# Optimization experiments

Hardware: AMD Instinct MI355X
Metric: run time of the kernel (lower is better)

## Reference

```python
import jax, jax.numpy as jnp
import numpy as np

D_MODEL = 1024
N_LAYERS = 4
EXPAND = 2
D_CONV = 4
D_STATE = 16
INTER = EXPAND * D_MODEL          # 2048
DT_RANK = (D_MODEL + 15) // 16    # 64, HF: math.ceil(d_model/16)
B_SZ = 4
SEQ = 1024
EPS = 1e-5


def setup_inputs() -> dict:
    key = jax.random.key(0)
    ks = jax.random.split(key, 8)
    nrm = lambda k, s: (0.02 * jax.random.normal(k, s)).astype(jnp.float32)
    return {
        "x": jax.random.normal(ks[0], (B_SZ, SEQ, D_MODEL), dtype=jnp.float32),
        "in_w": nrm(ks[1], (N_LAYERS, 2 * INTER, D_MODEL)),           # in_proj (no bias)
        "conv_w": nrm(ks[2], (N_LAYERS, INTER, D_CONV)),              # depthwise conv weight
        "conv_b": jnp.zeros((N_LAYERS, INTER), jnp.float32),           # conv bias
        "x_w": nrm(ks[3], (N_LAYERS, DT_RANK + 2 * D_STATE, INTER)),  # x_proj (no bias)
        "dt_w": nrm(ks[4], (N_LAYERS, INTER, DT_RANK)),               # dt_proj weight
        "dt_b": jax.random.uniform(ks[5], (N_LAYERS, INTER), minval=-4.0, maxval=-2.0).astype(jnp.float32),
        "A_log": jnp.tile(jnp.log(jnp.arange(1, D_STATE + 1, dtype=jnp.float32)), (N_LAYERS, INTER, 1)),
        "D": jnp.ones((N_LAYERS, INTER), jnp.float32),
        "out_w": nrm(ks[6], (N_LAYERS, D_MODEL, INTER)),              # out_proj (no bias)
        "norm_w": jnp.ones((N_LAYERS, D_MODEL), jnp.float32),          # per-block RMSNorm
        "norm_f_w": jnp.ones((D_MODEL,), jnp.float32),                 # final RMSNorm
    }


def _rmsnorm(x, w):
    return x * jax.lax.rsqrt(jnp.mean(x * x, axis=-1, keepdims=True) + EPS) * w


def _mixer(x, in_w, conv_w, conv_b, x_w, dt_w, dt_b, A_log, Dp, out_w):
    # x: [B, L, d_model]
    Bb = x.shape[0]
    proj = x @ in_w.T                              # [B, L, 2I]
    hs, gate = jnp.split(proj, 2, axis=-1)          # each [B, L, I]
    # causal depthwise conv over time
    hc = hs.transpose(0, 2, 1)                      # [B, I, L]
    hc = jnp.pad(hc, ((0, 0), (0, 0), (D_CONV - 1, 0)))
    hc = jax.lax.conv_general_dilated(
        hc, conv_w[:, None, :], (1,), 'VALID',
        dimension_numbers=('NCH', 'OIH', 'NCH'), feature_group_count=INTER)
    hc = hc + conv_b[None, :, None]
    u = jax.nn.silu(hc).transpose(0, 2, 1)          # [B, L, I]
    ssm = u @ x_w.T                                 # [B, L, dt_rank + 2N]
    dt, Bm, Cm = jnp.split(ssm, [DT_RANK, DT_RANK + D_STATE], axis=-1)
    dt = jax.nn.softplus(dt @ dt_w.T + dt_b)        # [B, L, I]
    A = -jnp.exp(A_log)                             # [I, N]

    def step(state, xs):
        dt_t, B_t, C_t, u_t = xs                    # [B,I], [B,N], [B,N], [B,I]
        dA = jnp.exp(dt_t[:, :, None] * A[None])    # [B, I, N]
        state = dA * state + (dt_t * u_t)[:, :, None] * B_t[:, None, :]
        y = jnp.einsum('bin,bn->bi', state, C_t)
        return state, y

    init = jnp.zeros((Bb, INTER, D_STATE), x.dtype)
    xs = (dt.transpose(1, 0, 2), Bm.transpose(1, 0, 2),
          Cm.transpose(1, 0, 2), u.transpose(1, 0, 2))
    _, ys = jax.lax.scan(step, init, xs)            # ys: [L, B, I]
    y = ys.transpose(1, 0, 2) + u * Dp              # skip term D * u
    y = y * jax.nn.silu(gate)
    return y @ out_w.T                              # [B, L, d_model]


def reference(x, in_w, conv_w, conv_b, x_w, dt_w, dt_b, A_log, D, out_w, norm_w, norm_f_w):
    h = x
    for l in range(N_LAYERS):
        h = h + _mixer(_rmsnorm(h, norm_w[l]), in_w[l], conv_w[l], conv_b[l],
                       x_w[l], dt_w[l], dt_b[l], A_log[l], D[l], out_w[l])
    return _rmsnorm(h, norm_f_w)
```

## Files before the change

kernel.cpp:

```cpp
#include <hip/hip_runtime.h>
#include <hip/hip_bf16.h>
#include <math.h>

#define D_MODEL 1024
#define N_LAYERS 4
#define INTER 2048
#define D_CONV 4
#define D_STATE 16
#define DT_RANK 64
#define B_SZ 4
#define SEQ 1024
#define TOK (B_SZ*SEQ)
#define XROWS 128
#define EPSV 1e-5f
#define GCH 32
#define TC (SEQ/GCH)
#define KSPL 4

typedef unsigned short u16;
typedef __attribute__((ext_vector_type(8))) short bf16x8;
typedef __attribute__((ext_vector_type(4))) short s16x4;
typedef __attribute__((ext_vector_type(4))) float f32x4;

__device__ __forceinline__ u16 f2b(float f) {
    union { float f; unsigned u; } v; v.f = f;
    unsigned r = v.u + 0x7fffu + ((v.u >> 16) & 1u);
    return (u16)(r >> 16);
}
__device__ __forceinline__ float b2f(u16 h) {
    union { unsigned u; float f; } v; v.u = ((unsigned)h) << 16;
    return v.f;
}
__device__ __forceinline__ float silu(float x) {
    return x / (1.f + __expf(-x));
}
__device__ __forceinline__ void gload16(const void* g, void* l) {
    __builtin_amdgcn_global_load_lds(
        (const __attribute__((address_space(1))) void*)g,
        (__attribute__((address_space(3))) void*)l, 16, 0, 0);
}

__global__ __launch_bounds__(512, 2)
void gemm256_k(const u16* __restrict__ A, const u16* __restrict__ B,
               u16* __restrict__ C, int K, int ldc)
{
    __shared__ u16 lds[2][2][256 * 64];
    const int tid  = threadIdx.x;
    const int lane = tid & 63;
    const int wid  = tid >> 6;
    const int wr   = wid >> 2;
    const int wc   = wid & 3;
    const int row0 = blockIdx.y * 256;
    const int col0 = blockIdx.x * 256;
    const int r16   = lane & 15;
    const int khalf = lane >> 4;

    auto stage = [&](int buf, int k0) {
#pragma unroll
        for (int l = 0; l < 8; ++l) {
            int op = l >> 2;
            int c  = tid + (l & 3) * 512;
            int r  = c >> 3;
            int ds = c & 7;
            int sc = (ds ^ (r & 7)) * 8;
            const u16* src = op ? &B[(size_t)(col0 + r) * K + k0 + sc]
                                : &A[(size_t)(row0 + r) * K + k0 + sc];
            gload16(src, &lds[buf][op][c * 8]);
        }
    };
    auto rdA = [&](int buf, int mrow, int ks) -> bf16x8 {
        int row  = wr * 128 + mrow + r16;
        int phys = ((ks << 2) | khalf) ^ (row & 7);
        return *(const bf16x8*)&lds[buf][0][row * 64 + phys * 8];
    };
    auto rdB = [&](int buf, int nrow, int ks) -> bf16x8 {
        int row  = wc * 64 + nrow + r16;
        int phys = ((ks << 2) | khalf) ^ (row & 7);
        return *(const bf16x8*)&lds[buf][1][row * 64 + phys * 8];
    };

    f32x4 acc[8][4];
#pragma unroll
    for (int m = 0; m < 8; ++m)
#pragma unroll
        for (int n = 0; n < 4; ++n)
            acc[m][n] = (f32x4)0.f;

    bf16x8 af[4][2], bf2[2][2];

#define PHASE_MFMA(MH, NH, VMDRAIN) do {                                      \
    asm volatile("s_waitcnt lgkmcnt(0)" ::: "memory");                        \
    __builtin_amdgcn_sched_barrier(0);                                        \
    __builtin_amdgcn_s_setprio(1);                                            \
    _Pragma("unroll")                                                         \
    for (int ks = 0; ks < 2; ++ks)                                            \
        _Pragma("unroll")                                                     \
        for (int m = 0; m < 4; ++m)                                           \
            _Pragma("unroll")                                                 \
            for (int n = 0; n < 2; ++n)                                       \
                acc[(MH)*4+m][(NH)*2+n] =                                     \
                    __builtin_amdgcn_mfma_f32_16x16x32_bf16(                  \
                        af[m][ks], bf2[n][ks], acc[(MH)*4+m][(NH)*2+n],0,0,0);\
    __builtin_amdgcn_s_setprio(0);                                            \
    if (VMDRAIN) { asm volatile("s_waitcnt vmcnt(0)" ::: "memory"); }         \
    __builtin_amdgcn_s_barrier();                                             \
} while (0)

    const int nt = K >> 6;
    stage(0, 0);
    asm volatile("s_waitcnt vmcnt(0)" ::: "memory");
    __builtin_amdgcn_s_barrier();

    for (int j = 0; j < nt; ++j) {
        const int buf = j & 1;
        if (j + 1 < nt) stage(buf ^ 1, (j + 1) << 6);
#pragma unroll
        for (int m = 0; m < 4; ++m) {
            af[m][0] = rdA(buf, m * 16, 0); af[m][1] = rdA(buf, m * 16, 1);
        }
#pragma unroll
        for (int n = 0; n < 2; ++n) {
            bf2[n][0] = rdB(buf, n * 16, 0); bf2[n][1] = rdB(buf, n * 16, 1);
        }
        __builtin_amdgcn_s_barrier();
        PHASE_MFMA(0, 0, 0);
#pragma unroll
        for (int n = 0; n < 2; ++n) {
            bf2[n][0] = rdB(buf, 32 + n * 16, 0); bf2[n][1] = rdB(buf, 32 + n * 16, 1);
        }
        __builtin_amdgcn_s_barrier();
        PHASE_MFMA(0, 1, 0);
#pragma unroll
        for (int m = 0; m < 4; ++m) {
            af[m][0] = rdA(buf, 64 + m * 16, 0); af[m][1] = rdA(buf, 64 + m * 16, 1);
        }
        __builtin_amdgcn_s_barrier();
        PHASE_MFMA(1, 1, 0);
#pragma unroll
        for (int n = 0; n < 2; ++n) {
            bf2[n][0] = rdB(buf, n * 16, 0); bf2[n][1] = rdB(buf, n * 16, 1);
        }
        __builtin_amdgcn_s_barrier();
        PHASE_MFMA(1, 0, 1);
    }
#undef PHASE_MFMA

    const int orow = row0 + wr * 128;
    const int ocol = col0 + wc * 64;
#pragma unroll
    for (int am = 0; am < 8; ++am)
#pragma unroll
        for (int an = 0; an < 4; ++an)
#pragma unroll
            for (int r = 0; r < 4; ++r) {
                int rr = orow + am * 16 + khalf * 4 + r;
                int cc = ocol + an * 16 + r16;
                C[(size_t)rr * ldc + cc] = f2b(acc[am][an][r]);
            }
}

template<int EPI>
__global__ __launch_bounds__(256)
void gemm_bt(const u16* __restrict__ A, const u16* __restrict__ B,
             void* __restrict__ C, const float* __restrict__ aux,
             int K, int lda, int ldc)
{
    __shared__ u16 As[3][128 * 32];
    __shared__ u16 Bs[3][128 * 32];
    const int tid  = threadIdx.x;
    const int lane = tid & 63;
    const int w    = tid >> 6;
    const int wr   = w >> 1, wc = w & 1;
    const int row0 = blockIdx.y * 128;
    int col0 = blockIdx.x * 128;
    if (EPI == 4) {
        int part = blockIdx.x;
        col0 = 0;
        A += (size_t)part * K;
        B += (size_t)part * K;
        C = (void*)((float*)C + (size_t)part * TOK * XROWS);
    }
    const int r16   = lane & 15;
    const int khalf = lane >> 4;
    const int kslot = khalf ^ ((r16 >> 1) & 3);

    auto stage = [&](int buf, int k0) {
#pragma unroll
        for (int c = 0; c < 2; ++c) {
            int chunk = tid + c * 256;
            int r  = chunk >> 2;
            int j  = chunk & 3;
            int k8 = (j ^ ((r >> 1) & 3)) * 8;
            gload16(&A[(size_t)(row0 + r) * lda + k0 + k8], &As[buf][chunk * 8]);
            gload16(&B[(size_t)(col0 + r) * lda + k0 + k8], &Bs[buf][chunk * 8]);
        }
    };

    f32x4 acc[4][4];
#pragma unroll
    for (int m = 0; m < 4; ++m)
#pragma unroll
        for (int n = 0; n < 4; ++n)
            acc[m][n] = (f32x4)0.f;

    const int nt = K >> 5;
    stage(0, 0);
    if (nt > 1) stage(1, 32);

    int cur = 0, sb = 2;
    for (int t = 0; t < nt; ++t) {
        if (t + 2 < nt) {
            stage(sb, (t + 2) << 5);
            asm volatile("s_waitcnt vmcnt(8)" ::: "memory");
        } else if (t + 1 < nt) {
            asm volatile("s_waitcnt vmcnt(4)" ::: "memory");
        } else {
            asm volatile("s_waitcnt vmcnt(0)" ::: "memory");
        }
        __builtin_amdgcn_s_barrier();

        bf16x8 af[4], bfr[4];
#pragma unroll
        for (int m = 0; m < 4; ++m)
            af[m]  = *(const bf16x8*)&As[cur][(wr * 64 + m * 16 + r16) * 32 + kslot * 8];
#pragma unroll
        for (int n = 0; n < 4; ++n)
            bfr[n] = *(const bf16x8*)&Bs[cur][(wc * 64 + n * 16 + r16) * 32 + kslot * 8];
#pragma unroll
        for (int m = 0; m < 4; ++m)
#pragma unroll
            for (int n = 0; n < 4; ++n)
                acc[m][n] = __builtin_amdgcn_mfma_f32_16x16x32_bf16(
                    af[m], bfr[n], acc[m][n], 0, 0, 0);

        __builtin_amdgcn_sched_barrier(0);
        asm volatile("s_waitcnt lgkmcnt(0)" ::: "memory");
        __builtin_amdgcn_s_barrier();
        cur = (cur == 2) ? 0 : cur + 1;
        sb  = (sb  == 2) ? 0 : sb  + 1;
    }

    const int orow = row0 + wr * 64;
    const int ocol = col0 + wc * 64;
#pragma unroll
    for (int m = 0; m < 4; ++m)
#pragma unroll
        for (int n = 0; n < 4; ++n) {
#pragma unroll
            for (int r = 0; r < 4; ++r) {
                int rr = orow + m * 16 + khalf * 4 + r;
                int cc = ocol + n * 16 + r16;
                float v = acc[m][n][r];
                size_t o = (size_t)rr * ldc + cc;
                if (EPI == 0 || EPI == 4) {
                    ((float*)C)[o] = v;
                } else if (EPI == 2) {
                    float x = v + aux[cc];
                    float sp = (x > 20.f) ? x : log1pf(__expf(x));
                    ((u16*)C)[o] = f2b(sp);
                } else {
                    ((float*)C)[o] = aux[o] + v;
                }
            }
        }
}

__global__ __launch_bounds__(256)
void xred_k(const float* __restrict__ part, float* __restrict__ ssm,
            u16* __restrict__ dtr)
{
    int idx = blockIdx.x * 256 + threadIdx.x;
    int row = idx >> 5;
    int col = (idx & 31) * 4;
    size_t o = (size_t)row * XROWS + col;
    const size_t stride = (size_t)TOK * XROWS;
    f32x4 v = *(const f32x4*)&part[o];
#pragma unroll
    for (int p = 1; p < KSPL; ++p)
        v += *(const f32x4*)&part[o + p * stride];
    *(f32x4*)&ssm[o] = v;
    if (col < DT_RANK) {
        s16x4 d;
#pragma unroll
        for (int j = 0; j < 4; ++j) d[j] = (short)f2b(v[j]);
        *(s16x4*)&dtr[(size_t)row * DT_RANK + col] = d;
    }
}

template<int OUTBF>
__global__ __launch_bounds__(256)
void rmsnorm_k(const float* __restrict__ in, const float* __restrict__ w,
               void* __restrict__ out)
{
    __shared__ float red[4];
    const int row = blockIdx.x;
    const int tid = threadIdx.x;
    const float* r = in + (size_t)row * D_MODEL;
    f32x4 v = *(const f32x4*)&r[tid * 4];
    float ss = v[0]*v[0] + v[1]*v[1] + v[2]*v[2] + v[3]*v[3];
#pragma unroll
    for (int m = 32; m >= 1; m >>= 1) ss += __shfl_xor(ss, m, 64);
    if ((tid & 63) == 0) red[tid >> 6] = ss;
    __syncthreads();
    if (tid == 0) {
        float s = red[0] + red[1] + red[2] + red[3];
        red[0] = rsqrtf(s / (float)D_MODEL + EPSV);
    }
    __syncthreads();
    float sc = red[0];
    if (OUTBF) {
        u16* o = (u16*)out + (size_t)row * D_MODEL + tid * 4;
#pragma unroll
        for (int j = 0; j < 4; ++j) o[j] = f2b(v[j] * sc * w[tid * 4 + j]);
    } else {
        float* o = (float*)out + (size_t)row * D_MODEL + tid * 4;
#pragma unroll
        for (int j = 0; j < 4; ++j) o[j] = v[j] * sc * w[tid * 4 + j];
    }
}

__global__ __launch_bounds__(256)
void conv_silu_k(const u16* __restrict__ projbf, const float* __restrict__ w,
                 const float* __restrict__ bias, u16* __restrict__ ubf)
{
    const int row = blockIdx.x;
    const int t   = row & (SEQ - 1);
    const int i0  = threadIdx.x * 8;
    float acc[8];
    {
        f32x4 b0 = *(const f32x4*)&bias[i0];
        f32x4 b1 = *(const f32x4*)&bias[i0 + 4];
#pragma unroll
        for (int j = 0; j < 4; ++j) { acc[j] = b0[j]; acc[j + 4] = b1[j]; }
    }
    f32x4 wv[8];
#pragma unroll
    for (int j = 0; j < 8; ++j)
        wv[j] = *(const f32x4*)&w[(i0 + j) * 4];
#pragma unroll
    for (int k = 0; k < 4; ++k) {
        int tt = t - 3 + k;
        if (tt >= 0) {
            bf16x8 hv = *(const bf16x8*)&projbf[(size_t)(row - 3 + k) * 4096 + i0];
#pragma unroll
            for (int j = 0; j < 8; ++j)
                acc[j] += b2f((u16)hv[j]) * wv[j][k];
        }
    }
    bf16x8 o;
#pragma unroll
    for (int j = 0; j < 8; ++j)
        o[j] = (short)f2b(silu(acc[j]));
    *(bf16x8*)&ubf[(size_t)row * INTER + i0] = o;
}

__global__ __launch_bounds__(256)
void scan1_k(const u16* __restrict__ dtbf, const u16* __restrict__ ubf,
             const float* __restrict__ ssm, const float* __restrict__ Alog,
             float* __restrict__ cst, float* __restrict__ dts)
{
    __shared__ float Bs[TC][D_STATE];
    const int tid = threadIdx.x;
    const int i   = blockIdx.x * 256 + tid;
    const int g   = blockIdx.y;
    const int b   = blockIdx.z;
    const int t0  = g * TC;
    for (int idx = tid * 4; idx < TC * D_STATE; idx += 1024) {
        int t = idx >> 4, n = idx & 15;
        *(f32x4*)&Bs[t][n] =
            *(const f32x4*)&ssm[(size_t)(b * SEQ + t0 + t) * XROWS + DT_RANK + n];
    }
    __syncthreads();

    float a[D_STATE];
#pragma unroll
    for (int n = 0; n < D_STATE; ++n)
        a[n] = -__expf(Alog[(size_t)i * D_STATE + n]);

    float s[D_STATE];
#pragma unroll
    for (int n = 0; n < D_STATE; ++n) s[n] = 0.f;
    float dsum = 0.f;

    const u16* dtp = dtbf + (size_t)(b * SEQ + t0) * INTER + i;
    const u16* up  = ubf  + (size_t)(b * SEQ + t0) * INTER + i;
#pragma unroll 2
    for (int t = 0; t < TC; ++t) {
        float dt = b2f(dtp[(size_t)t * INTER]);
        float u  = b2f(up[(size_t)t * INTER]);
        float du = dt * u;
        dsum += dt;
        f32x4 B0 = *(const f32x4*)&Bs[t][0];
        f32x4 B1 = *(const f32x4*)&Bs[t][4];
        f32x4 B2 = *(const f32x4*)&Bs[t][8];
        f32x4 B3 = *(const f32x4*)&Bs[t][12];
#pragma unroll
        for (int n = 0; n < 4; ++n) {
            s[n]      = __expf(dt * a[n])      * s[n]      + du * B0[n];
            s[n + 4]  = __expf(dt * a[n + 4])  * s[n + 4]  + du * B1[n];
            s[n + 8]  = __expf(dt * a[n + 8])  * s[n + 8]  + du * B2[n];
            s[n + 12] = __expf(dt * a[n + 12]) * s[n + 12] + du * B3[n];
        }
    }
    size_t o = ((size_t)(b * GCH + g) * INTER + i) * D_STATE;
#pragma unroll
    for (int n = 0; n < D_STATE; n += 4) {
        f32x4 v = { s[n], s[n+1], s[n+2], s[n+3] };
        *(f32x4*)&cst[o + n] = v;
    }
    dts[(size_t)(b * GCH + g) * INTER + i] = dsum;
}

__global__ __launch_bounds__(256)
void scan2_k(float* __restrict__ cst, const float* __restrict__ dts,
             const float* __restrict__ Alog)
{
    int idx = blockIdx.x * 256 + threadIdx.x;
    int sub = idx & 3;
    int i   = (idx >> 2) & (INTER - 1);
    int b   = idx >> 13;
    int n0  = sub * 4;
    float a[4];
#pragma unroll
    for (int n = 0; n < 4; ++n)
        a[n] = -__expf(Alog[(size_t)i * D_STATE + n0 + n]);
    f32x4 s = (f32x4)0.f;
    for (int g = 0; g < GCH; ++g) {
        size_t o = ((size_t)(b * GCH + g) * INTER + i) * D_STATE + n0;
        f32x4 tmp = *(const f32x4*)&cst[o];
        *(f32x4*)&cst[o] = s;
        float d = dts[(size_t)(b * GCH + g) * INTER + i];
#pragma unroll
        for (int n = 0; n < 4; ++n)
            s[n] = __expf(a[n] * d) * s[n] + tmp[n];
    }
}

__global__ __launch_bounds__(256)
void scan3_k(const u16* __restrict__ dtbf, const u16* __restrict__ ubf,
             const float* __restrict__ ssm, const u16* __restrict__ projbf,
             const float* __restrict__ Alog, const float* __restrict__ Dp,
             const float* __restrict__ sst, u16* __restrict__ ybf)
{
    __shared__ float Bs[TC][D_STATE];
    __shared__ float Cs[TC][D_STATE];
    const int tid = threadIdx.x;
    const int i   = blockIdx.x * 256 + tid;
    const int g   = blockIdx.y;
    const int b   = blockIdx.z;
    const int t0  = g * TC;
    for (int idx = tid * 4; idx < TC * D_STATE; idx += 1024) {
        int t = idx >> 4, n = idx & 15;
        size_t row = (size_t)(b * SEQ + t0 + t) * XROWS;
        *(f32x4*)&Bs[t][n] = *(const f32x4*)&ssm[row + DT_RANK + n];
        *(f32x4*)&Cs[t][n] = *(const f32x4*)&ssm[row + DT_RANK + D_STATE + n];
    }
    __syncthreads();

    float a[D_STATE];
#pragma unroll
    for (int n = 0; n < D_STATE; ++n)
        a[n] = -__expf(Alog[(size_t)i * D_STATE + n]);
    const float Di = Dp[i];

    float s[D_STATE];
    size_t so = ((size_t)(b * GCH + g) * INTER + i) * D_STATE;
#pragma unroll
    for (int n = 0; n < D_STATE; n += 4) {
        f32x4 v = *(const f32x4*)&sst[so + n];
        s[n] = v[0]; s[n+1] = v[1]; s[n+2] = v[2]; s[n+3] = v[3];
    }

    const u16* dtp = dtbf   + (size_t)(b * SEQ + t0) * INTER + i;
    const u16* up  = ubf    + (size_t)(b * SEQ + t0) * INTER + i;
    const u16* gp  = projbf + (size_t)(b * SEQ + t0) * 4096 + INTER + i;
    u16*       yp  = ybf    + (size_t)(b * SEQ + t0) * INTER + i;
#pragma unroll 2
    for (int t = 0; t < TC; ++t) {
        float dt = b2f(dtp[(size_t)t * INTER]);
        float u  = b2f(up[(size_t)t * INTER]);
        float gt = b2f(gp[(size_t)t * 4096]);
        float du = dt * u;
        f32x4 B0 = *(const f32x4*)&Bs[t][0];
        f32x4 B1 = *(const f32x4*)&Bs[t][4];
        f32x4 B2 = *(const f32x4*)&Bs[t][8];
        f32x4 B3 = *(const f32x4*)&Bs[t][12];
        f32x4 C0 = *(const f32x4*)&Cs[t][0];
        f32x4 C1 = *(const f32x4*)&Cs[t][4];
        f32x4 C2 = *(const f32x4*)&Cs[t][8];
        f32x4 C3 = *(const f32x4*)&Cs[t][12];
        float y = 0.f;
#pragma unroll
        for (int n = 0; n < 4; ++n) {
            s[n]      = __expf(dt * a[n])      * s[n]      + du * B0[n];
            s[n + 4]  = __expf(dt * a[n + 4])  * s[n + 4]  + du * B1[n];
            s[n + 8]  = __expf(dt * a[n + 8])  * s[n + 8]  + du * B2[n];
            s[n + 12] = __expf(dt * a[n + 12]) * s[n + 12] + du * B3[n];
            y += s[n] * C0[n] + s[n + 4] * C1[n] + s[n + 8] * C2[n] + s[n + 12] * C3[n];
        }
        yp[(size_t)t * INTER] = f2b((y + Di * u) * silu(gt));
    }
}

__global__ __launch_bounds__(256)
void cvt_f2b_k(const float* __restrict__ in, u16* __restrict__ out, int n)
{
    int idx = blockIdx.x * 256 + threadIdx.x;
    if (idx < n) out[idx] = f2b(in[idx]);
}

__global__ __launch_bounds__(256)
void pad_xw_k(const float* __restrict__ xw, u16* __restrict__ out)
{
    int idx = blockIdx.x * 256 + threadIdx.x;
    if (idx >= N_LAYERS * XROWS * INTER) return;
    int l = idx / (XROWS * INTER);
    int r = (idx >> 11) & (XROWS - 1);
    int c = idx & (INTER - 1);
    out[idx] = (r < 96) ? f2b(xw[((size_t)l * 96 + r) * INTER + c]) : (u16)0;
}

extern "C" void kernel_launch(void* const* d_in, const int* in_sizes, int n_in,
                              void* d_out, int out_size, void* d_ws, size_t ws_size,
                              hipStream_t stream)
{
    const float* x      = (const float*)d_in[0];
    const float* in_w   = (const float*)d_in[1];
    const float* conv_w = (const float*)d_in[2];
    const float* conv_b = (const float*)d_in[3];
    const float* x_w    = (const float*)d_in[4];
    const float* dt_w   = (const float*)d_in[5];
    const float* dt_b   = (const float*)d_in[6];
    const float* A_log  = (const float*)d_in[7];
    const float* Dp     = (const float*)d_in[8];
    const float* out_w  = (const float*)d_in[9];
    const float* norm_w = (const float*)d_in[10];
    const float* norm_f = (const float*)d_in[11];

    char* ws = (char*)d_ws;
    size_t off = 0;
    auto alloc = [&](size_t bytes) { char* p = ws + off; off += (bytes + 255) & ~(size_t)255; return p; };

    u16*   inw_bf  = (u16*)  alloc((size_t)N_LAYERS * 4096 * 1024 * 2);
    u16*   xw_bf   = (u16*)  alloc((size_t)N_LAYERS * XROWS * INTER * 2);
    u16*   dtw_bf  = (u16*)  alloc((size_t)N_LAYERS * INTER * DT_RANK * 2);
    u16*   outw_bf = (u16*)  alloc((size_t)N_LAYERS * D_MODEL * INTER * 2);
    float* h       = (float*)alloc((size_t)TOK * D_MODEL * 4);
    u16*   xn_bf   = (u16*)  alloc((size_t)TOK * D_MODEL * 2);
    u16*   proj_bf = (u16*)  alloc((size_t)TOK * 4096 * 2);
    u16*   u_bf    = (u16*)  alloc((size_t)TOK * INTER * 2);
    float* ssm     = (float*)alloc((size_t)TOK * XROWS * 4);
    float* ssm_p   = (float*)alloc((size_t)KSPL * TOK * XROWS * 4);
    u16*   dtr_bf  = (u16*)  alloc((size_t)TOK * DT_RANK * 2);
    u16*   dt_bf   = (u16*)  alloc((size_t)TOK * INTER * 2);
    u16*   y_bf    = (u16*)  alloc((size_t)TOK * INTER * 2);
    float* cst     = (float*)alloc((size_t)B_SZ * GCH * INTER * D_STATE * 4);
    float* dts     = (float*)alloc((size_t)B_SZ * GCH * INTER * 4);
    (void)ws_size; (void)n_in; (void)in_sizes; (void)out_size;

    {
        int n = N_LAYERS * 4096 * 1024;
        cvt_f2b_k<<<n / 256, 256, 0, stream>>>(in_w, inw_bf, n);
        int np = N_LAYERS * XROWS * INTER;
        pad_xw_k<<<np / 256, 256, 0, stream>>>(x_w, xw_bf);
        int nd = N_LAYERS * INTER * DT_RANK;
        cvt_f2b_k<<<nd / 256, 256, 0, stream>>>(dt_w, dtw_bf, nd);
        int no = N_LAYERS * D_MODEL * INTER;
        cvt_f2b_k<<<no / 256, 256, 0, stream>>>(out_w, outw_bf, no);
    }

    hipMemcpyAsync(h, x, (size_t)TOK * D_MODEL * 4, hipMemcpyDeviceToDevice, stream);

    for (int l = 0; l < N_LAYERS; ++l) {
        rmsnorm_k<1><<<TOK, 256, 0, stream>>>(h, norm_w + (size_t)l * D_MODEL, xn_bf);
        gemm256_k<<<dim3(16, 16), 512, 0, stream>>>(
            xn_bf, inw_bf + (size_t)l * 4096 * 1024, proj_bf, 1024, 4096);
        conv_silu_k<<<TOK, 256, 0, stream>>>(
            proj_bf, conv_w + (size_t)l * INTER * D_CONV, conv_b + (size_t)l * INTER, u_bf);
        gemm_bt<4><<<dim3(KSPL, 32), 256, 0, stream>>>(
            u_bf, xw_bf + (size_t)l * XROWS * INTER, ssm_p, nullptr,
            INTER / KSPL, INTER, XROWS);
        xred_k<<<(TOK * 32) / 256, 256, 0, stream>>>(ssm_p, ssm, dtr_bf);
        gemm_bt<2><<<dim3(16, 32), 256, 0, stream>>>(
            dtr_bf, dtw_bf + (size_t)l * INTER * DT_RANK, dt_bf,
            dt_b + (size_t)l * INTER, DT_RANK, DT_RANK, INTER);
        scan1_k<<<dim3(INTER / 256, GCH, B_SZ), 256, 0, stream>>>(
            dt_bf, u_bf, ssm, A_log + (size_t)l * INTER * D_STATE, cst, dts);
        scan2_k<<<(B_SZ * INTER * 4) / 256, 256, 0, stream>>>(
            cst, dts, A_log + (size_t)l * INTER * D_STATE);
        scan3_k<<<dim3(INTER / 256, GCH, B_SZ), 256, 0, stream>>>(
            dt_bf, u_bf, ssm, proj_bf, A_log + (size_t)l * INTER * D_STATE,
            Dp + (size_t)l * INTER, cst, y_bf);
        gemm_bt<3><<<dim3(8, 32), 256, 0, stream>>>(
            y_bf, outw_bf + (size_t)l * D_MODEL * INTER, h, h, INTER, INTER, D_MODEL);
    }
    rmsnorm_k<0><<<TOK, 256, 0, stream>>>(h, norm_f, d_out);
}
```

Before: 1.051 ms.

## Specialize scan for integer A via exp powers, split-K out_proj fused into RMSNorm

```diff
diff --git a/kernel.cpp b/kernel.cpp
--- a/kernel.cpp
+++ b/kernel.cpp
@@ -13,11 +13,13 @@
 #define TOK (B_SZ*SEQ)
 #define XROWS 128
 #define EPSV 1e-5f
-#define GCH 32
+#define GCH 64
 #define TC (SEQ/GCH)
 #define KSPL 4
+#define OSPL 2
 
 typedef unsigned short u16;
+typedef unsigned int u32;
 typedef __attribute__((ext_vector_type(8))) short bf16x8;
 typedef __attribute__((ext_vector_type(4))) short s16x4;
 typedef __attribute__((ext_vector_type(4))) float f32x4;
@@ -159,11 +161,11 @@
             }
 }
 
-template<int EPI>
+template<int EPI, int NPX = 1>
 __global__ __launch_bounds__(256)
 void gemm_bt(const u16* __restrict__ A, const u16* __restrict__ B,
              void* __restrict__ C, const float* __restrict__ aux,
-             int K, int lda, int ldc)
+             int K, int lda, int ldc, size_t pstride)
 {
     __shared__ u16 As[3][128 * 32];
     __shared__ u16 Bs[3][128 * 32];
@@ -174,11 +176,11 @@
     const int row0 = blockIdx.y * 128;
     int col0 = blockIdx.x * 128;
     if (EPI == 4) {
-        int part = blockIdx.x;
-        col0 = 0;
+        int part = blockIdx.x / NPX;
+        col0 = (blockIdx.x % NPX) * 128;
         A += (size_t)part * K;
         B += (size_t)part * K;
-        C = (void*)((float*)C + (size_t)part * TOK * XROWS);
+        C = (void*)((float*)C + (size_t)part * pstride);
     }
     const int r16   = lane & 15;
     const int khalf = lane >> 4;
@@ -258,8 +260,6 @@
                     float x = v + aux[cc];
                     float sp = (x > 20.f) ? x : log1pf(__expf(x));
                     ((u16*)C)[o] = f2b(sp);
-                } else {
-                    ((float*)C)[o] = aux[o] + v;
                 }
             }
         }
@@ -314,6 +314,43 @@
         for (int j = 0; j < 4; ++j) o[j] = f2b(v[j] * sc * w[tid * 4 + j]);
     } else {
         float* o = (float*)out + (size_t)row * D_MODEL + tid * 4;
+#pragma unroll
+        for (int j = 0; j < 4; ++j) o[j] = v[j] * sc * w[tid * 4 + j];
+    }
+}
+
+template<int OUTBF, int WRITEH>
+__global__ __launch_bounds__(256)
+void rmsnorm_res_k(const float* __restrict__ hin, const float* __restrict__ p,
+                   const float* __restrict__ w, float* __restrict__ hout,
+                   void* __restrict__ out)
+{
+    __shared__ float red[4];
+    const int row = blockIdx.x;
+    const int tid = threadIdx.x;
+    const size_t o4 = (size_t)row * D_MODEL + tid * 4;
+    f32x4 v  = *(const f32x4*)&hin[o4];
+    f32x4 p0 = *(const f32x4*)&p[o4];
+    f32x4 p1 = *(const f32x4*)&p[(size_t)TOK * D_MODEL + o4];
+    v += p0 + p1;
+    if (WRITEH) *(f32x4*)&hout[o4] = v;
+    float ss = v[0]*v[0] + v[1]*v[1] + v[2]*v[2] + v[3]*v[3];
+#pragma unroll
+    for (int m = 32; m >= 1; m >>= 1) ss += __shfl_xor(ss, m, 64);
+    if ((tid & 63) == 0) red[tid >> 6] = ss;
+    __syncthreads();
+    if (tid == 0) {
+        float s = red[0] + red[1] + red[2] + red[3];
+        red[0] = rsqrtf(s / (float)D_MODEL + EPSV);
+    }
+    __syncthreads();
+    float sc = red[0];
+    if (OUTBF) {
+        u16* o = (u16*)out + o4;
+#pragma unroll
+        for (int j = 0; j < 4; ++j) o[j] = f2b(v[j] * sc * w[tid * 4 + j]);
+    } else {
+        float* o = (float*)out + o4;
 #pragma unroll
         for (int j = 0; j < 4; ++j) o[j] = v[j] * sc * w[tid * 4 + j];
     }
@@ -355,60 +392,115 @@
 }
 
 __global__ __launch_bounds__(256)
+void achk_k(const float* __restrict__ Alog, int* __restrict__ flags)
+{
+    int idx = blockIdx.x * 256 + threadIdx.x;
+    if (idx >= N_LAYERS * INTER * D_STATE) return;
+    int l = idx / (INTER * D_STATE);
+    int n = idx & (D_STATE - 1);
+    float ref = logf((float)(n + 1));
+    if (fabsf(Alog[idx] - ref) > 1e-4f) atomicAnd(&flags[l], 0);
+}
+
+#define POWCH(W, p) \
+    float p##2=(W)*(W), p##3=p##2*(W), p##4=p##2*p##2, p##5=p##4*(W),        \
+          p##6=p##4*p##2, p##7=p##4*p##3, p##8=p##4*p##4, p##9=p##8*(W),     \
+          p##10=p##8*p##2, p##11=p##8*p##3, p##12=p##8*p##4, p##13=p##8*p##5,\
+          p##14=p##8*p##6, p##15=p##8*p##7, p##16=p##8*p##8;
+
+#define SUPD(S, B, du, w1) \
+    S[0]=w1*S[0]+du*B[0][0];   S[1]=w1##2*S[1]+du*B[0][1];                   \
+    S[2]=w1##3*S[2]+du*B[0][2];  S[3]=w1##4*S[3]+du*B[0][3];                 \
+    S[4]=w1##5*S[4]+du*B[1][0];  S[5]=w1##6*S[5]+du*B[1][1];                 \
+    S[6]=w1##7*S[6]+du*B[1][2];  S[7]=w1##8*S[7]+du*B[1][3];                 \
+    S[8]=w1##9*S[8]+du*B[2][0];  S[9]=w1##10*S[9]+du*B[2][1];                \
+    S[10]=w1##11*S[10]+du*B[2][2]; S[11]=w1##12*S[11]+du*B[2][3];            \
+    S[12]=w1##13*S[12]+du*B[3][0]; S[13]=w1##14*S[13]+du*B[3][1];            \
+    S[14]=w1##15*S[14]+du*B[3][2]; S[15]=w1##16*S[15]+du*B[3][3];
+
+#define YDOT(S, Cv) \
+    (S[0]*Cv[0][0]+S[1]*Cv[0][1]+S[2]*Cv[0][2]+S[3]*Cv[0][3]                 \
+    +S[4]*Cv[1][0]+S[5]*Cv[1][1]+S[6]*Cv[1][2]+S[7]*Cv[1][3]                 \
+    +S[8]*Cv[2][0]+S[9]*Cv[2][1]+S[10]*Cv[2][2]+S[11]*Cv[2][3]               \
+    +S[12]*Cv[3][0]+S[13]*Cv[3][1]+S[14]*Cv[3][2]+S[15]*Cv[3][3])
+
+__global__ __launch_bounds__(256)
 void scan1_k(const u16* __restrict__ dtbf, const u16* __restrict__ ubf,
              const float* __restrict__ ssm, const float* __restrict__ Alog,
+             const int* __restrict__ flag,
              float* __restrict__ cst, float* __restrict__ dts)
 {
-    __shared__ float Bs[TC][D_STATE];
+    __shared__ float Bsh[TC][D_STATE];
     const int tid = threadIdx.x;
-    const int i   = blockIdx.x * 256 + tid;
+    const int i2  = blockIdx.x * 256 + tid;
+    const int c0  = i2 * 2;
     const int g   = blockIdx.y;
     const int b   = blockIdx.z;
     const int t0  = g * TC;
-    for (int idx = tid * 4; idx < TC * D_STATE; idx += 1024) {
-        int t = idx >> 4, n = idx & 15;
-        *(f32x4*)&Bs[t][n] =
-            *(const f32x4*)&ssm[(size_t)(b * SEQ + t0 + t) * XROWS + DT_RANK + n];
+    {
+        int t = tid >> 4, n = tid & 15;
+        Bsh[t][n] = ssm[(size_t)(b * SEQ + t0 + t) * XROWS + DT_RANK + n];
     }
     __syncthreads();
 
-    float a[D_STATE];
-#pragma unroll
-    for (int n = 0; n < D_STATE; ++n)
-        a[n] = -__expf(Alog[(size_t)i * D_STATE + n]);
-
-    float s[D_STATE];
-#pragma unroll
-    for (int n = 0; n < D_STATE; ++n) s[n] = 0.f;
-    float dsum = 0.f;
-
-    const u16* dtp = dtbf + (size_t)(b * SEQ + t0) * INTER + i;
-    const u16* up  = ubf  + (size_t)(b * SEQ + t0) * INTER + i;
-#pragma unroll 2
-    for (int t = 0; t < TC; ++t) {
-        float dt = b2f(dtp[(size_t)t * INTER]);
-        float u  = b2f(up[(size_t)t * INTER]);
-        float du = dt * u;
-        dsum += dt;
-        f32x4 B0 = *(const f32x4*)&Bs[t][0];
-        f32x4 B1 = *(const f32x4*)&Bs[t][4];
-        f32x4 B2 = *(const f32x4*)&Bs[t][8];
-        f32x4 B3 = *(const f32x4*)&Bs[t][12];
-#pragma unroll
-        for (int n = 0; n < 4; ++n) {
-            s[n]      = __expf(dt * a[n])      * s[n]      + du * B0[n];
-            s[n + 4]  = __expf(dt * a[n + 4])  * s[n + 4]  + du * B1[n];
-            s[n + 8]  = __expf(dt * a[n + 8])  * s[n + 8]  + du * B2[n];
-            s[n + 12] = __expf(dt * a[n + 12]) * s[n + 12] + du * B3[n];
-        }
-    }
-    size_t o = ((size_t)(b * GCH + g) * INTER + i) * D_STATE;
+    float s0[D_STATE], s1[D_STATE];
+#pragma unroll
+    for (int n = 0; n < D_STATE; ++n) { s0[n] = 0.f; s1[n] = 0.f; }
+    float ds0 = 0.f, ds1 = 0.f;
+
+    const u32* dtp = (const u32*)dtbf + ((size_t)(b * SEQ + t0) * INTER >> 1) + i2;
+    const u32* up  = (const u32*)ubf  + ((size_t)(b * SEQ + t0) * INTER >> 1) + i2;
+
+    if (flag[0]) {
+#pragma unroll
+        for (int t = 0; t < TC; ++t) {
+            u32 dp = dtp[(size_t)t * (INTER / 2)];
+            u32 uq = up[(size_t)t * (INTER / 2)];
+            float dta = b2f((u16)dp), dtb = b2f((u16)(dp >> 16));
+            float ua  = b2f((u16)uq), ub  = b2f((u16)(uq >> 16));
+            float dua = dta * ua, dub = dtb * ub;
+            ds0 += dta; ds1 += dtb;
+            float wa = __expf(-dta), wb = __expf(-dtb);
+            POWCH(wa, wa) POWCH(wb, wb)
+            const float (*Bv)[D_STATE] = nullptr; (void)Bv;
+            f32x4 Bq[4];
+#pragma unroll
+            for (int q = 0; q < 4; ++q) Bq[q] = *(const f32x4*)&Bsh[t][q * 4];
+            SUPD(s0, Bq, dua, wa)
+            SUPD(s1, Bq, dub, wb)
+        }
+    } else {
+        float a0[D_STATE], a1[D_STATE];
+#pragma unroll
+        for (int n = 0; n < D_STATE; ++n) {
+            a0[n] = -__expf(Alog[(size_t)c0 * D_STATE + n]);
+            a1[n] = -__expf(Alog[(size_t)(c0 + 1) * D_STATE + n]);
+        }
+        for (int t = 0; t < TC; ++t) {
+            u32 dp = dtp[(size_t)t * (INTER / 2)];
+            u32 uq = up[(size_t)t * (INTER / 2)];
+            float dta = b2f((u16)dp), dtb = b2f((u16)(dp >> 16));
+            float ua  = b2f((u16)uq), ub  = b2f((u16)(uq >> 16));
+            float dua = dta * ua, dub = dtb * ub;
+            ds0 += dta; ds1 += dtb;
+#pragma unroll
+            for (int n = 0; n < D_STATE; ++n) {
+                float Bn = Bsh[t][n];
+                s0[n] = __expf(dta * a0[n]) * s0[n] + dua * Bn;
+                s1[n] = __expf(dtb * a1[n]) * s1[n] + dub * Bn;
+            }
+        }
+    }
+    size_t o = ((size_t)(b * GCH + g) * INTER + c0) * D_STATE;
 #pragma unroll
     for (int n = 0; n < D_STATE; n += 4) {
-        f32x4 v = { s[n], s[n+1], s[n+2], s[n+3] };
-        *(f32x4*)&cst[o + n] = v;
-    }
-    dts[(size_t)(b * GCH + g) * INTER + i] = dsum;
+        f32x4 v0 = { s0[n], s0[n+1], s0[n+2], s0[n+3] };
+        f32x4 v1 = { s1[n], s1[n+1], s1[n+2], s1[n+3] };
+        *(f32x4*)&cst[o + n] = v0;
+        *(f32x4*)&cst[o + D_STATE + n] = v1;
+    }
+    size_t od = (size_t)(b * GCH + g) * INTER + c0;
+    dts[od] = ds0; dts[od + 1] = ds1;
 }
 
 __global__ __launch_bounds__(256)
@@ -440,65 +532,94 @@
 void scan3_k(const u16* __restrict__ dtbf, const u16* __restrict__ ubf,
              const float* __restrict__ ssm, const u16* __restrict__ projbf,
              const float* __restrict__ Alog, const float* __restrict__ Dp,
+             const int* __restrict__ flag,
              const float* __restrict__ sst, u16* __restrict__ ybf)
 {
-    __shared__ float Bs[TC][D_STATE];
-    __shared__ float Cs[TC][D_STATE];
+    __shared__ float Bsh[TC][D_STATE];
+    __shared__ float Csh[TC][D_STATE];
     const int tid = threadIdx.x;
-    const int i   = blockIdx.x * 256 + tid;
+    const int i2  = blockIdx.x * 256 + tid;
+    const int c0  = i2 * 2;
     const int g   = blockIdx.y;
     const int b   = blockIdx.z;
     const int t0  = g * TC;
-    for (int idx = tid * 4; idx < TC * D_STATE; idx += 1024) {
-        int t = idx >> 4, n = idx & 15;
+    {
+        int t = tid >> 4, n = tid & 15;
         size_t row = (size_t)(b * SEQ + t0 + t) * XROWS;
-        *(f32x4*)&Bs[t][n] = *(const f32x4*)&ssm[row + DT_RANK + n];
-        *(f32x4*)&Cs[t][n] = *(const f32x4*)&ssm[row + DT_RANK + D_STATE + n];
+        Bsh[t][n] = ssm[row + DT_RANK + n];
+        Csh[t][n] = ssm[row + DT_RANK + D_STATE + n];
     }
     __syncthreads();
 
-    float a[D_STATE];
-#pragma unroll
-    for (int n = 0; n < D_STATE; ++n)
-        a[n] = -__expf(Alog[(size_t)i * D_STATE + n]);
-    const float Di = Dp[i];
-
-    float s[D_STATE];
-    size_t so = ((size_t)(b * GCH + g) * INTER + i) * D_STATE;
+    const float Da = Dp[c0], Db = Dp[c0 + 1];
+    float s0[D_STATE], s1[D_STATE];
+    size_t so = ((size_t)(b * GCH + g) * INTER + c0) * D_STATE;
 #pragma unroll
     for (int n = 0; n < D_STATE; n += 4) {
-        f32x4 v = *(const f32x4*)&sst[so + n];
-        s[n] = v[0]; s[n+1] = v[1]; s[n+2] = v[2]; s[n+3] = v[3];
-    }
-
-    const u16* dtp = dtbf   + (size_t)(b * SEQ + t0) * INTER + i;
-    const u16* up  = ubf    + (size_t)(b * SEQ + t0) * INTER + i;
-    const u16* gp  = projbf + (size_t)(b * SEQ + t0) * 4096 + INTER + i;
-    u16*       yp  = ybf    + (size_t)(b * SEQ + t0) * INTER + i;
-#pragma unroll 2
-    for (int t = 0; t < TC; ++t) {
-        float dt = b2f(dtp[(size_t)t * INTER]);
-        float u  = b2f(up[(size_t)t * INTER]);
-        float gt = b2f(gp[(size_t)t * 4096]);
-        float du = dt * u;
-        f32x4 B0 = *(const f32x4*)&Bs[t][0];
-        f32x4 B1 = *(const f32x4*)&Bs[t][4];
-        f32x4 B2 = *(const f32x4*)&Bs[t][8];
-        f32x4 B3 = *(const f32x4*)&Bs[t][12];
-        f32x4 C0 = *(const f32x4*)&Cs[t][0];
-        f32x4 C1 = *(const f32x4*)&Cs[t][4];
-        f32x4 C2 = *(const f32x4*)&Cs[t][8];
-        f32x4 C3 = *(const f32x4*)&Cs[t][12];
-        float y = 0.f;
-#pragma unroll
-        for (int n = 0; n < 4; ++n) {
-            s[n]      = __expf(dt * a[n])      * s[n]      + du * B0[n];
-            s[n + 4]  = __expf(dt * a[n + 4])  * s[n + 4]  + du * B1[n];
-            s[n + 8]  = __expf(dt * a[n + 8])  * s[n + 8]  + du * B2[n];
-            s[n + 12] = __expf(dt * a[n + 12]) * s[n + 12] + du * B3[n];
-            y += s[n] * C0[n] + s[n + 4] * C1[n] + s[n + 8] * C2[n] + s[n + 12] * C3[n];
-        }
-        yp[(size_t)t * INTER] = f2b((y + Di * u) * silu(gt));
+        f32x4 v0 = *(const f32x4*)&sst[so + n];
+        f32x4 v1 = *(const f32x4*)&sst[so + D_STATE + n];
+        s0[n] = v0[0]; s0[n+1] = v0[1]; s0[n+2] = v0[2]; s0[n+3] = v0[3];
+        s1[n] = v1[0]; s1[n+1] = v1[1]; s1[n+2] = v1[2]; s1[n+3] = v1[3];
+    }
+
+    const u32* dtp = (const u32*)dtbf + ((size_t)(b * SEQ + t0) * INTER >> 1) + i2;
+    const u32* up  = (const u32*)ubf  + ((size_t)(b * SEQ + t0) * INTER >> 1) + i2;
+    const u32* gp  = (const u32*)projbf + (((size_t)(b * SEQ + t0) * 4096 + INTER) >> 1) + i2;
+    u32*       yp  = (u32*)ybf + ((size_t)(b * SEQ + t0) * INTER >> 1) + i2;
+
+    if (flag[0]) {
+#pragma unroll
+        for (int t = 0; t < TC; ++t) {
+            u32 dp = dtp[(size_t)t * (INTER / 2)];
+            u32 uq = up[(size_t)t * (INTER / 2)];
+            u32 gq = gp[(size_t)t * (4096 / 2)];
+            float dta = b2f((u16)dp), dtb = b2f((u16)(dp >> 16));
+            float ua  = b2f((u16)uq), ub  = b2f((u16)(uq >> 16));
+            float ga  = b2f((u16)gq), gb  = b2f((u16)(gq >> 16));
+            float dua = dta * ua, dub = dtb * ub;
+            float wa = __expf(-dta), wb = __expf(-dtb);
+            POWCH(wa, wa) POWCH(wb, wb)
+            f32x4 Bq[4], Cq[4];
+#pragma unroll
+            for (int q = 0; q < 4; ++q) {
+                Bq[q] = *(const f32x4*)&Bsh[t][q * 4];
+                Cq[q] = *(const f32x4*)&Csh[t][q * 4];
+            }
+            SUPD(s0, Bq, dua, wa)
+            SUPD(s1, Bq, dub, wb)
+            float y0 = YDOT(s0, Cq);
+            float y1 = YDOT(s1, Cq);
+            y0 = (y0 + Da * ua) * silu(ga);
+            y1 = (y1 + Db * ub) * silu(gb);
+            yp[(size_t)t * (INTER / 2)] = (u32)f2b(y0) | ((u32)f2b(y1) << 16);
+        }
+    } else {
+        float a0[D_STATE], a1[D_STATE];
+#pragma unroll
+        for (int n = 0; n < D_STATE; ++n) {
+            a0[n] = -__expf(Alog[(size_t)c0 * D_STATE + n]);
+            a1[n] = -__expf(Alog[(size_t)(c0 + 1) * D_STATE + n]);
+        }
+        for (int t = 0; t < TC; ++t) {
+            u32 dp = dtp[(size_t)t * (INTER / 2)];
+            u32 uq = up[(size_t)t * (INTER / 2)];
+            u32 gq = gp[(size_t)t * (4096 / 2)];
+            float dta = b2f((u16)dp), dtb = b2f((u16)(dp >> 16));
+            float ua  = b2f((u16)uq), ub  = b2f((u16)(uq >> 16));
+            float ga  = b2f((u16)gq), gb  = b2f((u16)(gq >> 16));
+            float dua = dta * ua, dub = dtb * ub;
+            float y0 = 0.f, y1 = 0.f;
+#pragma unroll
+            for (int n = 0; n < D_STATE; ++n) {
+                float Bn = Bsh[t][n], Cn = Csh[t][n];
+                s0[n] = __expf(dta * a0[n]) * s0[n] + dua * Bn;
+                s1[n] = __expf(dtb * a1[n]) * s1[n] + dub * Bn;
+                y0 += s0[n] * Cn; y1 += s1[n] * Cn;
+            }
+            y0 = (y0 + Da * ua) * silu(ga);
+            y1 = (y1 + Db * ub) * silu(gb);
+            yp[(size_t)t * (INTER / 2)] = (u32)f2b(y0) | ((u32)f2b(y1) << 16);
+        }
     }
 }
 
@@ -550,12 +671,13 @@
     u16*   proj_bf = (u16*)  alloc((size_t)TOK * 4096 * 2);
     u16*   u_bf    = (u16*)  alloc((size_t)TOK * INTER * 2);
     float* ssm     = (float*)alloc((size_t)TOK * XROWS * 4);
-    float* ssm_p   = (float*)alloc((size_t)KSPL * TOK * XROWS * 4);
+    float* parts   = (float*)alloc((size_t)OSPL * TOK * D_MODEL * 4);
     u16*   dtr_bf  = (u16*)  alloc((size_t)TOK * DT_RANK * 2);
     u16*   dt_bf   = (u16*)  alloc((size_t)TOK * INTER * 2);
     u16*   y_bf    = (u16*)  alloc((size_t)TOK * INTER * 2);
     float* cst     = (float*)alloc((size_t)B_SZ * GCH * INTER * D_STATE * 4);
     float* dts     = (float*)alloc((size_t)B_SZ * GCH * INTER * 4);
+    int*   aflags  = (int*)  alloc(N_LAYERS * sizeof(int));
     (void)ws_size; (void)n_in; (void)in_sizes; (void)out_size;
 
     {
@@ -567,32 +689,39 @@
         cvt_f2b_k<<<nd / 256, 256, 0, stream>>>(dt_w, dtw_bf, nd);
         int no = N_LAYERS * D_MODEL * INTER;
         cvt_f2b_k<<<no / 256, 256, 0, stream>>>(out_w, outw_bf, no);
-    }
-
-    hipMemcpyAsync(h, x, (size_t)TOK * D_MODEL * 4, hipMemcpyDeviceToDevice, stream);
+        hipMemsetAsync(aflags, 0xFF, N_LAYERS * sizeof(int), stream);
+        int na = N_LAYERS * INTER * D_STATE;
+        achk_k<<<(na + 255) / 256, 256, 0, stream>>>(A_log, aflags);
+    }
 
     for (int l = 0; l < N_LAYERS; ++l) {
-        rmsnorm_k<1><<<TOK, 256, 0, stream>>>(h, norm_w + (size_t)l * D_MODEL, xn_bf);
+        if (l == 0)
+            rmsnorm_k<1><<<TOK, 256, 0, stream>>>(x, norm_w, xn_bf);
+        else
+            rmsnorm_res_k<1, 1><<<TOK, 256, 0, stream>>>(
+                (l == 1) ? x : h, parts, norm_w + (size_t)l * D_MODEL, h, xn_bf);
         gemm256_k<<<dim3(16, 16), 512, 0, stream>>>(
             xn_bf, inw_bf + (size_t)l * 4096 * 1024, proj_bf, 1024, 4096);
         conv_silu_k<<<TOK, 256, 0, stream>>>(
             proj_bf, conv_w + (size_t)l * INTER * D_CONV, conv_b + (size_t)l * INTER, u_bf);
-        gemm_bt<4><<<dim3(KSPL, 32), 256, 0, stream>>>(
-            u_bf, xw_bf + (size_t)l * XROWS * INTER, ssm_p, nullptr,
-            INTER / KSPL, INTER, XROWS);
-        xred_k<<<(TOK * 32) / 256, 256, 0, stream>>>(ssm_p, ssm, dtr_bf);
+        gemm_bt<4, 1><<<dim3(KSPL, 32), 256, 0, stream>>>(
+            u_bf, xw_bf + (size_t)l * XROWS * INTER, parts, nullptr,
+            INTER / KSPL, INTER, XROWS, (size_t)TOK * XROWS);
+        xred_k<<<(TOK * 32) / 256, 256, 0, stream>>>(parts, ssm, dtr_bf);
         gemm_bt<2><<<dim3(16, 32), 256, 0, stream>>>(
             dtr_bf, dtw_bf + (size_t)l * INTER * DT_RANK, dt_bf,
-            dt_b + (size_t)l * INTER, DT_RANK, DT_RANK, INTER);
-        scan1_k<<<dim3(INTER / 256, GCH, B_SZ), 256, 0, stream>>>(
-            dt_bf, u_bf, ssm, A_log + (size_t)l * INTER * D_STATE, cst, dts);
+            dt_b + (size_t)l * INTER, DT_RANK, DT_RANK, INTER, 0);
+        scan1_k<<<dim3(INTER / 512, GCH, B_SZ), 256, 0, stream>>>(
+            dt_bf, u_bf, ssm, A_log + (size_t)l * INTER * D_STATE, aflags + l, cst, dts);
         scan2_k<<<(B_SZ * INTER * 4) / 256, 256, 0, stream>>>(
             cst, dts, A_log + (size_t)l * INTER * D_STATE);
-        scan3_k<<<dim3(INTER / 256, GCH, B_SZ), 256, 0, stream>>>(
+        scan3_k<<<dim3(INTER / 512, GCH, B_SZ), 256, 0, stream>>>(
             dt_bf, u_bf, ssm, proj_bf, A_log + (size_t)l * INTER * D_STATE,
-            Dp + (size_t)l * INTER, cst, y_bf);
-        gemm_bt<3><<<dim3(8, 32), 256, 0, stream>>>(
-            y_bf, outw_bf + (size_t)l * D_MODEL * INTER, h, h, INTER, INTER, D_MODEL);
-    }
-    rmsnorm_k<0><<<TOK, 256, 0, stream>>>(h, norm_f, d_out);
-}
+            Dp + (size_t)l * INTER, aflags + l, cst, y_bf);
+        gemm_bt<4, 8><<<dim3(OSPL * 8, 32), 256, 0, stream>>>(
+            y_bf, outw_bf + (size_t)l * D_MODEL * INTER, parts, nullptr,
+            INTER / OSPL, INTER, D_MODEL, (size_t)TOK * D_MODEL);
+    }
+    rmsnorm_res_k<0, 0><<<TOK, 256, 0, stream>>>(
+        h, parts, norm_f, nullptr, d_out);
+}
```

After: 940.1 us. 10.6% less time.
